# Optimization experiments

Hardware: AMD Instinct MI355X
Metric: run time of the kernel (lower is better)

Reference implementation:

```python
import jax, jax.numpy as jnp
import numpy as np

NEG = -10000.0
SINK = 16  # first 16 keys are always-attended sink tokens


def setup_inputs() -> dict:
    key = jax.random.key(0)
    k0, k1, k2 = jax.random.split(key, 3)
    B, H, KH, S, D = 1, 16, 4, 2048, 128
    return {
        "query": jax.random.normal(k0, (B, H, S, D), dtype=jnp.float32),
        "key_t": jax.random.normal(k1, (B, KH, S, D), dtype=jnp.float32),
        "value": jax.random.normal(k2, (B, KH, S, D), dtype=jnp.float32),
        "lsh_threshold": jnp.full((KH,), 70.0, dtype=jnp.float32),
        "top_k": 64,
        "window_size": 128,
    }


def reference(query, key_t, value, lsh_threshold, top_k, window_size):
    # query: [B,H,S,D]; key_t/value: [B,KH,S,D] (GQA, QH = H//KH)
    B, H, S, D = query.shape
    KH = key_t.shape[1]
    QH = H // KH
    q = query.reshape(B, KH, QH, S, D)

    # LSH sign-bit matching count. packbits64(x>=0) + (D - xor_popcount) ==
    # number of positions where sign(q)==sign(k) == (D + <sgn(q),sgn(k)>)/2.
    qs = jnp.where(q >= 0, 1.0, -1.0).astype(jnp.float32)
    ksgn = jnp.where(key_t >= 0, 1.0, -1.0).astype(jnp.float32)
    match = (D + jnp.einsum('bkqsd,bkld->bkqsl', qs, ksgn)) * 0.5  # [B,KH,QH,S,S]
    # max over the QH group (dim=2, keepdim) then compare against per-KV-head threshold
    lsh_mask = match.max(axis=2, keepdims=True) > lsh_threshold.reshape(1, KH, 1, 1, 1)

    qi = jnp.arange(S)[:, None]
    ki = jnp.arange(S)[None, :]
    causal = qi >= ki                                             # [S,S]
    window = ((jnp.abs(qi - ki) < window_size) | (ki < SINK)) & causal

    mask = causal & lsh_mask                                      # [B,KH,QH,S,S]

    scale = 1.0 / jnp.sqrt(jnp.asarray(D, jnp.float32))
    scores = jnp.einsum('bkqsd,bkld->bkqsl', q, key_t) * scale    # [B,KH,QH,S,S]
    scores = jnp.where(jnp.logical_not(mask) & jnp.logical_not(window), NEG, scores)

    # long-term candidates: exclude the local window, then take top_k per query row
    scores_lt = jnp.where(window, NEG, scores)
    _, idx = jax.lax.top_k(scores_lt, top_k)                      # [B,KH,QH,S,top_k]
    topk_mask = jnp.put_along_axis(
        jnp.zeros(scores.shape, dtype=bool), idx, True, axis=-1, inplace=False)

    both = window | topk_mask
    probs = jax.nn.softmax(jnp.where(both, scores, NEG), axis=-1)
    out = jnp.einsum('bkqsl,bkld->bskqd', probs, value)           # [B,S,KH,QH,D]
    return out.reshape(B, S, H * D)
```

## Files before the change

### kernel.cpp

```cpp
#include <hip/hip_runtime.h>

#define S_LEN   2048
#define D_DIM   128
#define KH_N    4
#define QH_N    4
#define H_N     (KH_N * QH_N)
#define SINK_N  16
#define SB_N    4
#define NREG    16
#define CHUNK   512
#define NCH     4
#define PLANE32 260
#define SCR32   672
#define TIECAP  672

typedef __attribute__((ext_vector_type(8))) _Float16 f16x8;
typedef __attribute__((ext_vector_type(2))) _Float16 f16x2;
typedef __attribute__((ext_vector_type(4))) float f32x4;

__device__ __forceinline__ void lds_fence() {
  asm volatile("s_waitcnt lgkmcnt(0)" ::: "memory");
}
__device__ __forceinline__ unsigned short f2h(float f) {
  _Float16 h = (_Float16)f;
  return __builtin_bit_cast(unsigned short, h);
}
__device__ __forceinline__ unsigned int pkrtz_u32(float a, float b) {
  return __builtin_bit_cast(unsigned int, __builtin_amdgcn_cvt_pkrtz(a, b));
}
__device__ __forceinline__ unsigned int pack_okey16(float a, float b) {
  unsigned int u = pkrtz_u32(a, b);
  unsigned int t = (u >> 15) & 0x00010001u;
  return u ^ ((t * 0x7FFFu) | 0x80008000u);
}
__device__ __forceinline__ float okinv16(unsigned int k) {
  unsigned short bits = (k & 0x8000u) ? (unsigned short)(k & 0x7FFFu)
                                      : (unsigned short)(~k & 0xFFFFu);
  return (float)__builtin_bit_cast(_Float16, bits);
}

__global__ __launch_bounds__(256) void pack_kernel(
    const float* __restrict__ k, const float* __restrict__ v,
    unsigned long long* __restrict__ signs,
    unsigned short* __restrict__ kf16, unsigned int* __restrict__ vf16) {
  const int wid  = (blockIdx.x * 256 + threadIdx.x) >> 6;
  const int lane = threadIdx.x & 63;
  const int rbase = wid * 4;
  const int KROWS = KH_N * S_LEN;

  if (rbase < KROWS) {
    const float* src = k + (size_t)rbase * D_DIM;
    float a[4], b[4];
#pragma unroll
    for (int r = 0; r < 4; r++) {
      a[r] = src[r * D_DIM + lane];
      b[r] = src[r * D_DIM + 64 + lane];
    }
#pragma unroll
    for (int r = 0; r < 4; r++) {
      unsigned long long b0 = __ballot(a[r] >= 0.0f);
      unsigned long long b1 = __ballot(b[r] >= 0.0f);
      if (lane == 0) {
        signs[(size_t)(rbase + r) * 2]     = b0;
        signs[(size_t)(rbase + r) * 2 + 1] = b1;
      }
      unsigned short* rb = kf16 + (size_t)(rbase + r) * 128;
      rb[lane]      = f2h(a[r]);
      rb[64 + lane] = f2h(b[r]);
    }
  } else {
    int vr = rbase - KROWS;
    const float* src = v + (size_t)vr * D_DIM;
    float2 f2[4];
#pragma unroll
    for (int r = 0; r < 4; r++)
      f2[r] = *(const float2*)(src + r * D_DIM + lane * 2);
#pragma unroll
    for (int r = 0; r < 4; r++) {
      unsigned int pk = (unsigned int)f2h(f2[r].x) |
                        ((unsigned int)f2h(f2[r].y) << 16);
      vf16[(size_t)(vr + r) * 64 + lane] = pk;
    }
  }
}

__global__ __launch_bounds__(512, 4) void attn_kernel(
    const float* __restrict__ query, const float* __restrict__ thr,
    const int* __restrict__ p_topk, const int* __restrict__ p_wsz,
    const unsigned long long* __restrict__ signs,
    const unsigned short* __restrict__ kf16,
    const unsigned int* __restrict__ vf16,
    float* __restrict__ out) {
  const int xcd  = blockIdx.x & 7;
  const int kh   = xcd >> 1;
  const int g    = ((blockIdx.x >> 3) << 1) | (xcd & 1);
  const int sb   = (511 - g) << 2;
  const int tid  = threadIdx.x;
  const int lane = tid & 63;
  const int w    = tid >> 6;
  const int col  = lane & 15;
  const int quad = lane >> 4;
  const int s_off = w >> 1;
  const int part  = w & 1;

  __shared__ __align__(16) unsigned int   buf[16 * PLANE32];
  __shared__ __align__(16) unsigned int   scr[8][SCR32];
  __shared__ __align__(16) unsigned short q_f16[16][136];
  __shared__ unsigned long long mask_sh[SB_N][32];
  __shared__ unsigned long long qs_sh[16][2];
  __shared__ int ncand_sh[SB_N];

  const int   topk   = *p_topk;
  const int   wsz    = *p_wsz;
  const float thresh = thr[kh];
  const float scale  = 0.088388347648318447f;

  const int s_w     = sb + s_off;
  const int nrows_w = s_w + 1;
  int wlo_w = s_w - (wsz - 1); if (wlo_w < 0) wlo_w = 0;
  const int lt_hi_w = s_w - wsz;
  const int imax_w  = (nrows_w + 127) >> 7;
  const int smax    = sb + 3;
  const int nrows_pad = (smax + 1 + 15) & ~15;

#pragma unroll
  for (int v = 0; v < 4; v++) {
    int r = v * 4 + (tid >> 7);
    int d = tid & 127;
    float f = query[((size_t)(kh * QH_N + (r & 3)) * S_LEN
                     + (sb + (r >> 2))) * D_DIM + d];
    unsigned long long b = __ballot(f >= 0.0f);
    if (lane == 0) qs_sh[v * 4 + (w >> 1)][w & 1] = b;
    q_f16[r][d] = f2h(f * scale);
  }
  if (tid < 128) mask_sh[tid >> 5][tid & 31] = 0ull;
  if (tid < SB_N) ncand_sh[tid] = 0;
  __syncthreads();

  {
    unsigned long long a0[4], a1[4];
#pragma unroll
    for (int q2 = 0; q2 < 4; q2++) {
      a0[q2] = qs_sh[s_off * 4 + q2][0];
      a1[q2] = qs_sh[s_off * 4 + q2][1];
    }
    const unsigned long long* ksg = signs + (size_t)kh * S_LEN * 2;
    int cnt = 0;
    for (int l0 = part * 64; l0 <= lt_hi_w; l0 += 128) {
      int l = l0 + lane;
      bool match = false;
      if (l >= SINK_N && l <= lt_hi_w) {
        ulonglong2 kk = *(const ulonglong2*)(ksg + 2 * l);
        int best = 0;
#pragma unroll
        for (int q2 = 0; q2 < 4; q2++) {
          int m = 128 - __popcll(a0[q2] ^ kk.x) - __popcll(a1[q2] ^ kk.y);
          best = best > m ? best : m;
        }
        match = ((float)best > thresh);
      }
      unsigned long long m = __ballot(match);
      if (lane == 0) mask_sh[s_off][l0 >> 6] = m;
      cnt += (int)__popcll(m);
    }
    if (lane == 0 && cnt) atomicAdd(&ncand_sh[s_off], cnt);
  }

  f16x8 bfrag[4];
#pragma unroll
  for (int ks = 0; ks < 4; ks++)
    bfrag[ks] = *(const f16x8*)&q_f16[col][ks * 32 + quad * 8];

  const unsigned short* kf_h = kf16 + ((size_t)kh << 11) * 128;
  unsigned int creg[2][NREG];
#pragma unroll
  for (int hq = 0; hq < 2; hq++)
#pragma unroll
    for (int i = 0; i < NREG; i++) creg[hq][i] = 0u;

#pragma unroll
  for (int cb = 0; cb < NCH; cb++) {
    int cbase = cb * CHUNK;
    int chunk_n = nrows_pad - cbase;
    if (chunk_n > CHUNK) chunk_n = CHUNK;
    if (chunk_n > 0) {
      int ntiles = chunk_n >> 4;
      for (int t = w; t < ntiles; t += 8) {
        int tb = cbase + t * 16;
        const unsigned char* ab =
            (const unsigned char*)(kf_h + (size_t)(tb + col) * 128) + quad * 16;
        f16x8 a0 = *(const f16x8*)(ab + 0);
        f16x8 a1 = *(const f16x8*)(ab + 64);
        f16x8 a2 = *(const f16x8*)(ab + 128);
        f16x8 a3 = *(const f16x8*)(ab + 192);
        f32x4 acc = {0.f, 0.f, 0.f, 0.f};
        acc = __builtin_amdgcn_mfma_f32_16x16x32_f16(a0, bfrag[0], acc, 0, 0, 0);
        acc = __builtin_amdgcn_mfma_f32_16x16x32_f16(a1, bfrag[1], acc, 0, 0, 0);
        acc = __builtin_amdgcn_mfma_f32_16x16x32_f16(a2, bfrag[2], acc, 0, 0, 0);
        acc = __builtin_amdgcn_mfma_f32_16x16x32_f16(a3, bfrag[3], acc, 0, 0, 0);
        unsigned int k01 = pack_okey16(acc[0], acc[1]);
        unsigned int k23 = pack_okey16(acc[2], acc[3]);
        int off = ((tb - cbase) >> 1) + quad * 2;
        buf[col * PLANE32 + off]     = k01;
        buf[col * PLANE32 + off + 1] = k23;
      }
    }
    __syncthreads();
    if (chunk_n > 0) {
#pragma unroll
      for (int hq = 0; hq < 2; hq++)
#pragma unroll
        for (int j2 = 0; j2 < 4; j2++) {
          int m = j2 * 64 + lane;
          if (2 * m < chunk_n)
            creg[hq][cb * 4 + j2] = buf[(2 * w + hq) * PLANE32 + m];
        }
    }
    __syncthreads();
  }

  unsigned int mybits = 0;
#pragma unroll
  for (int i = 0; i < NREG; i++) {
    if (i >= imax_w) break;
    unsigned long long wd = mask_sh[s_off][2 * i + (lane >> 5)];
    mybits |= ((unsigned int)((wd >> ((2 * lane) & 63)) & 3ull)) << (2 * i);
  }
  const int nc = ncand_sh[s_off];
  const bool selAll = (nc <= topk);

  unsigned int*       histw = &scr[w][0];
  unsigned long long* selq  = (unsigned long long*)&scr[w][256];
  unsigned int*       tls   = &scr[w][0];

  const int sub = lane & 15;
  const int quarter = lane >> 4;
  const uint4* vb4 = (const uint4*)(vf16 + ((size_t)kh << 11) * 64);

#pragma unroll
  for (int hq = 0; hq < 2; hq++) {
    const int qh = 2 * part + hq;

    unsigned int mx16 = 0;
#pragma unroll
    for (int i = 0; i < NREG; i++) {
      if (i >= imax_w) break;
      unsigned int u = creg[hq][i];
      int e0 = i * 128 + 2 * lane;
      unsigned int h0 = u & 0xFFFFu, h1 = u >> 16;
      if (e0 < nrows_w && h0 > mx16) mx16 = h0;
      if (e0 + 1 < nrows_w && h1 > mx16) mx16 = h1;
    }
#pragma unroll
    for (int off = 32; off > 0; off >>= 1) {
      unsigned int t = __shfl_down(mx16, off);
      mx16 = t > mx16 ? t : mx16;
    }
    mx16 = __shfl(mx16, 0);
    const float mxf = okinv16(mx16);

    unsigned int tkey = 0;
    bool useTie = false;
    int l_cut = S_LEN;
    if (!selAll) {
      unsigned int prefix = 0;
      int want = topk;
      unsigned int ceq = 0;
#pragma unroll
      for (int pass = 0; pass < 2; pass++) {
        int sh = 8 - pass * 8;
        {
          uint4 z = {0u, 0u, 0u, 0u};
          *(uint4*)&histw[lane * 4] = z;
        }
        lds_fence();
#pragma unroll
        for (int i = 0; i < NREG; i++) {
          if (i >= imax_w) break;
          unsigned int u = creg[hq][i];
          unsigned int b2 = (mybits >> (2 * i)) & 3u;
          if (b2 & 1u) {
            unsigned int key = u & 0xFFFFu;
            if ((pass == 0) || ((key >> 8) == prefix))
              atomicAdd(&histw[(key >> sh) & 255u], 1u);
          }
          if (b2 & 2u) {
            unsigned int key = u >> 16;
            if ((pass == 0) || ((key >> 8) == prefix))
              atomicAdd(&histw[(key >> sh) & 255u], 1u);
          }
        }
        lds_fence();
        uint4 cc = *(const uint4*)&histw[lane * 4];
        unsigned int c0 = cc.x, c1 = cc.y, c2 = cc.z, c3 = cc.w;
        unsigned int S3 = c3, S2 = c2 + S3, S1 = c1 + S2, S0 = c0 + S1;
        unsigned int tot = S0;
        unsigned int suf = tot;
#pragma unroll
        for (int off = 1; off < 64; off <<= 1) {
          unsigned int t = __shfl_down(suf, off);
          if (lane + off < 64) suf += t;
        }
        unsigned long long mk = __ballot(suf >= (unsigned int)want);
        int L = 63 - __clzll(mk);
        unsigned int se = suf - tot;
        unsigned int s3 = S3 + se, s2 = S2 + se, s1 = S1 + se, s0 = S0 + se;
        int j; unsigned int above, csel;
        unsigned int w2 = (unsigned int)want;
        if (s3 >= w2)      { j = 3; above = s3 - c3; csel = c3; }
        else if (s2 >= w2) { j = 2; above = s2 - c2; csel = c2; }
        else if (s1 >= w2) { j = 1; above = s1 - c1; csel = c1; }
        else               { j = 0; above = s0 - c0; csel = c0; }
        int d_me = (lane << 2) | j;
        int wp_me = want - (int)above;
        int digit = __shfl(d_me, L);
        want = __shfl(wp_me, L);
        ceq = (unsigned int)__shfl((int)csel, L);
        prefix = (prefix << 8) | (unsigned int)digit;
      }
      tkey = prefix;
      int rem = want;
      if ((int)ceq > rem) {
        useTie = true;
        if ((int)ceq <= TIECAP) {
          int tb = 0;
#pragma unroll
          for (int i = 0; i < NREG; i++) {
            if (i >= imax_w) break;
            unsigned int u = creg[hq][i];
            unsigned int b2 = (mybits >> (2 * i)) & 3u;
            int e0 = i * 128 + 2 * lane;
#pragma unroll
            for (int h2 = 0; h2 < 2; h2++) {
              bool tied = false;
              if (b2 & (1u << h2)) {
                unsigned int key = h2 ? (u >> 16) : (u & 0xFFFFu);
                tied = (key == tkey);
              }
              unsigned long long m = __ballot(tied);
              if (tied) {
                int pos = tb + __popcll(m & ((1ull << lane) - 1ull));
                tls[pos] = (unsigned int)(e0 + h2);
              }
              tb += (int)__popcll(m);
            }
          }
          lds_fence();
          unsigned int lcut = (unsigned int)S_LEN;
          for (int i2 = lane; i2 < (int)ceq; i2 += 64) {
            unsigned int v2 = tls[i2];
            int rank = 0;
            for (int j3 = 0; j3 < (int)ceq; j3++) rank += (tls[j3] < v2);
            if (rank == rem - 1) lcut = v2;
          }
#pragma unroll
          for (int off = 32; off > 0; off >>= 1) {
            unsigned int t = __shfl_down(lcut, off);
            lcut = t < lcut ? t : lcut;
          }
          l_cut = (int)__shfl((int)lcut, 0);
        } else {
          int lo = SINK_N, hi = lt_hi_w;
          while (lo < hi) {
            int mid = (lo + hi) >> 1;
            int cn = 0;
#pragma unroll
            for (int i = 0; i < NREG; i++) {
              if (i >= imax_w) break;
              unsigned int u = creg[hq][i];
              unsigned int b2 = (mybits >> (2 * i)) & 3u;
              int e0 = i * 128 + 2 * lane;
#pragma unroll
              for (int h2 = 0; h2 < 2; h2++) {
                if (b2 & (1u << h2)) {
                  unsigned int key = h2 ? (u >> 16) : (u & 0xFFFFu);
                  cn += (key == tkey && (e0 + h2) <= mid);
                }
              }
            }
#pragma unroll
            for (int off = 32; off > 0; off >>= 1) cn += __shfl_down(cn, off);
            cn = __shfl(cn, 0);
            if (cn >= rem) hi = mid; else lo = mid + 1;
          }
          l_cut = lo;
        }
      }
    }

    float sum = 0.0f;
    int bse = 0;
#pragma unroll
    for (int i = 0; i < NREG; i++) {
      if (i >= imax_w) break;
      unsigned int u = creg[hq][i];
      int e0 = i * 128 + 2 * lane;
#pragma unroll
      for (int h2 = 0; h2 < 2; h2++) {
        int e = e0 + h2;
        bool act = false;
        float p = 0.f;
        if (e < nrows_w) {
          unsigned int key = h2 ? (u >> 16) : (u & 0xFFFFu);
          bool inc = (e < SINK_N) || (e >= wlo_w);
          if (!inc && ((mybits >> (2 * i + h2)) & 1u))
            inc = selAll || (key > tkey) ||
                  (key == tkey && (!useTie || e <= l_cut));
          if (inc) { act = true; p = __expf(okinv16(key) - mxf); sum += p; }
        }
        unsigned long long m = __ballot(act);
        if (act) {
          int pi = bse + __popcll(m & ((1ull << lane) - 1ull));
          selq[pi] = ((unsigned long long)e << 32) |
                     (unsigned long long)__float_as_uint(p);
        }
        bse += (int)__popcll(m);
      }
    }
#pragma unroll
    for (int off = 32; off > 0; off >>= 1) sum += __shfl_down(sum, off);
    sum = __shfl(sum, 0);
    float rinv = 1.0f / sum;

    int nsel = bse;
    int nsel16 = (nsel + 15) & ~15;
    if (lane < nsel16 - nsel) selq[nsel + lane] = 0ull;
    lds_fence();

    float av[8] = {0.f, 0.f, 0.f, 0.f, 0.f, 0.f, 0.f, 0.f};
    for (int e = 0; e < nsel16; e += 16) {
      const unsigned long long* sq = &selq[e + 4 * quarter];
      ulonglong2 spA = *(const ulonglong2*)(sq);
      ulonglong2 spB = *(const ulonglong2*)(sq + 2);
      int l0 = (int)(spA.x >> 32), l1 = (int)(spA.y >> 32);
      int l2 = (int)(spB.x >> 32), l3 = (int)(spB.y >> 32);
      uint4 v0 = vb4[(size_t)l0 * 16 + sub];
      uint4 v1 = vb4[(size_t)l1 * 16 + sub];
      uint4 v2 = vb4[(size_t)l2 * 16 + sub];
      uint4 v3 = vb4[(size_t)l3 * 16 + sub];
      f16x2 phA = __builtin_bit_cast(
          f16x2, pkrtz_u32(__uint_as_float((unsigned int)spA.x),
                           __uint_as_float((unsigned int)spA.y)));
      f16x2 phB = __builtin_bit_cast(
          f16x2, pkrtz_u32(__uint_as_float((unsigned int)spB.x),
                           __uint_as_float((unsigned int)spB.y)));
#define DOT2P(va, vb, ph, comp, i0, i1)                                       \
      {                                                                       \
        unsigned int lo_ = __builtin_amdgcn_perm(vb.comp, va.comp, 0x05040100u); \
        unsigned int hi_ = __builtin_amdgcn_perm(vb.comp, va.comp, 0x07060302u); \
        av[i0] = __builtin_amdgcn_fdot2(__builtin_bit_cast(f16x2, lo_), ph,   \
                                        av[i0], false);                       \
        av[i1] = __builtin_amdgcn_fdot2(__builtin_bit_cast(f16x2, hi_), ph,   \
                                        av[i1], false);                       \
      }
      DOT2P(v0, v1, phA, x, 0, 1) DOT2P(v0, v1, phA, y, 2, 3)
      DOT2P(v0, v1, phA, z, 4, 5) DOT2P(v0, v1, phA, w, 6, 7)
      DOT2P(v2, v3, phB, x, 0, 1) DOT2P(v2, v3, phB, y, 2, 3)
      DOT2P(v2, v3, phB, z, 4, 5) DOT2P(v2, v3, phB, w, 6, 7)
#undef DOT2P
    }
#pragma unroll
    for (int d = 0; d < 8; d++) {
      av[d] += __shfl_xor(av[d], 16);
      av[d] += __shfl_xor(av[d], 32);
    }
    if (lane < 16) {
      size_t o = (size_t)s_w * (H_N * D_DIM)
               + (size_t)(kh * QH_N + qh) * D_DIM + (size_t)sub * 8;
      f32x4 r0 = {av[0] * rinv, av[1] * rinv, av[2] * rinv, av[3] * rinv};
      f32x4 r1 = {av[4] * rinv, av[5] * rinv, av[6] * rinv, av[7] * rinv};
      __builtin_nontemporal_store(r0, (f32x4*)(out + o));
      __builtin_nontemporal_store(r1, (f32x4*)(out + o + 4));
    }
    lds_fence();
  }
}

extern "C" void kernel_launch(void* const* d_in, const int* in_sizes, int n_in,
                              void* d_out, int out_size, void* d_ws, size_t ws_size,
                              hipStream_t stream) {
  const float* query = (const float*)d_in[0];
  const float* key   = (const float*)d_in[1];
  const float* value = (const float*)d_in[2];
  const float* thr   = (const float*)d_in[3];
  const int* p_topk  = (const int*)d_in[4];
  const int* p_wsz   = (const int*)d_in[5];
  float* out = (float*)d_out;

  char* ws = (char*)d_ws;
  unsigned long long* signs = (unsigned long long*)ws;
  unsigned short* kf16 = (unsigned short*)(ws + (size_t)KH_N * S_LEN * 16);
  unsigned int* vf16 = (unsigned int*)(ws + (size_t)KH_N * S_LEN * 16
                                          + (size_t)KH_N * S_LEN * 256);

  pack_kernel<<<1024, 256, 0, stream>>>(key, value, signs, kf16, vf16);

  attn_kernel<<<KH_N * (S_LEN / SB_N), 512, 0, stream>>>(
      query, thr, p_topk, p_wsz, signs, kf16, vf16, out);
}
```

Before: 275.9 us.

## Stage V chunks in LDS and gather selected rows from shared memory

Selected (index, prob) pairs are packed into 32-bit entries (16-bit index, fp16 prob), and per-128-row chunk offsets are recorded. The block then cooperatively stages each 128-row V chunk into LDS and every wave accumulates both query heads from the staged chunk. This replaces scattered global V gathers with coalesced loads that are shared across waves. It adds block-wide barriers per chunk, loads chunks that may be only sparsely used, lowers the tie-list cap and rounds the probabilities to fp16 earlier.

```diff
diff --git a/kernel.cpp b/kernel.cpp
--- a/kernel.cpp
+++ b/kernel.cpp
@@ -12,7 +12,7 @@
 #define NCH     4
 #define PLANE32 260
 #define SCR32   672
-#define TIECAP  672
+#define TIECAP  256
 
 typedef __attribute__((ext_vector_type(8))) _Float16 f16x8;
 typedef __attribute__((ext_vector_type(2))) _Float16 f16x2;
@@ -103,11 +103,12 @@
   const int s_off = w >> 1;
   const int part  = w & 1;
 
-  __shared__ __align__(16) unsigned int   buf[16 * PLANE32];
+  __shared__ __align__(16) unsigned int   big[8192];
   __shared__ __align__(16) unsigned int   scr[8][SCR32];
   __shared__ __align__(16) unsigned short q_f16[16][136];
   __shared__ unsigned long long mask_sh[SB_N][32];
   __shared__ unsigned long long qs_sh[16][2];
+  __shared__ unsigned short cse_sh[8][2][NREG + 1];
   __shared__ int ncand_sh[SB_N];
 
   const int   topk   = *p_topk;
@@ -201,8 +202,8 @@
         unsigned int k01 = pack_okey16(acc[0], acc[1]);
         unsigned int k23 = pack_okey16(acc[2], acc[3]);
         int off = ((tb - cbase) >> 1) + quad * 2;
-        buf[col * PLANE32 + off]     = k01;
-        buf[col * PLANE32 + off + 1] = k23;
+        big[col * PLANE32 + off]     = k01;
+        big[col * PLANE32 + off + 1] = k23;
       }
     }
     __syncthreads();
@@ -213,7 +214,7 @@
         for (int j2 = 0; j2 < 4; j2++) {
           int m = j2 * 64 + lane;
           if (2 * m < chunk_n)
-            creg[hq][cb * 4 + j2] = buf[(2 * w + hq) * PLANE32 + m];
+            creg[hq][cb * 4 + j2] = big[(2 * w + hq) * PLANE32 + m];
         }
     }
     __syncthreads();
@@ -229,17 +230,13 @@
   const int nc = ncand_sh[s_off];
   const bool selAll = (nc <= topk);
 
-  unsigned int*       histw = &scr[w][0];
-  unsigned long long* selq  = (unsigned long long*)&scr[w][256];
-  unsigned int*       tls   = &scr[w][0];
-
-  const int sub = lane & 15;
-  const int quarter = lane >> 4;
-  const uint4* vb4 = (const uint4*)(vf16 + ((size_t)kh << 11) * 64);
+  unsigned int* histw = &scr[w][0];
+
+  float rinv[2];
 
 #pragma unroll
   for (int hq = 0; hq < 2; hq++) {
-    const int qh = 2 * part + hq;
+    unsigned int* selq_h = &scr[w][256 + hq * 208];
 
     unsigned int mx16 = 0;
 #pragma unroll
@@ -323,6 +320,7 @@
       if ((int)ceq > rem) {
         useTie = true;
         if ((int)ceq <= TIECAP) {
+          unsigned int* tls = histw;
           int tb = 0;
 #pragma unroll
           for (int i = 0; i < NREG; i++) {
@@ -393,6 +391,7 @@
 #pragma unroll
     for (int i = 0; i < NREG; i++) {
       if (i >= imax_w) break;
+      if (lane == 0) cse_sh[w][hq][i] = (unsigned short)bse;
       unsigned int u = creg[hq][i];
       int e0 = i * 128 + 2 * lane;
 #pragma unroll
@@ -411,68 +410,91 @@
         unsigned long long m = __ballot(act);
         if (act) {
           int pi = bse + __popcll(m & ((1ull << lane) - 1ull));
-          selq[pi] = ((unsigned long long)e << 32) |
-                     (unsigned long long)__float_as_uint(p);
+          selq_h[pi] = ((unsigned int)e << 16) | (unsigned int)f2h(p);
         }
         bse += (int)__popcll(m);
       }
+    }
+    if (lane == 0) {
+      for (int i = imax_w; i <= NREG; i++)
+        cse_sh[w][hq][i] = (unsigned short)bse;
     }
 #pragma unroll
     for (int off = 32; off > 0; off >>= 1) sum += __shfl_down(sum, off);
     sum = __shfl(sum, 0);
-    float rinv = 1.0f / sum;
-
-    int nsel = bse;
-    int nsel16 = (nsel + 15) & ~15;
-    if (lane < nsel16 - nsel) selq[nsel + lane] = 0ull;
-    lds_fence();
-
-    float av[8] = {0.f, 0.f, 0.f, 0.f, 0.f, 0.f, 0.f, 0.f};
-    for (int e = 0; e < nsel16; e += 16) {
-      const unsigned long long* sq = &selq[e + 4 * quarter];
-      ulonglong2 spA = *(const ulonglong2*)(sq);
-      ulonglong2 spB = *(const ulonglong2*)(sq + 2);
-      int l0 = (int)(spA.x >> 32), l1 = (int)(spA.y >> 32);
-      int l2 = (int)(spB.x >> 32), l3 = (int)(spB.y >> 32);
-      uint4 v0 = vb4[(size_t)l0 * 16 + sub];
-      uint4 v1 = vb4[(size_t)l1 * 16 + sub];
-      uint4 v2 = vb4[(size_t)l2 * 16 + sub];
-      uint4 v3 = vb4[(size_t)l3 * 16 + sub];
-      f16x2 phA = __builtin_bit_cast(
-          f16x2, pkrtz_u32(__uint_as_float((unsigned int)spA.x),
-                           __uint_as_float((unsigned int)spA.y)));
-      f16x2 phB = __builtin_bit_cast(
-          f16x2, pkrtz_u32(__uint_as_float((unsigned int)spB.x),
-                           __uint_as_float((unsigned int)spB.y)));
+    rinv[hq] = 1.0f / sum;
+  }
+
+  const int sub = lane & 15;
+  const int quarter = lane >> 4;
+  const int nch_blk = (smax >> 7) + 1;
+  uint4* vstage = (uint4*)big;
+  const uint4* vsrc = (const uint4*)(vf16 + ((size_t)kh << 11) * 64);
+  float av[2][8];
+#pragma unroll
+  for (int hq = 0; hq < 2; hq++)
+#pragma unroll
+    for (int d = 0; d < 8; d++) av[hq][d] = 0.f;
+
+  for (int ch = 0; ch < nch_blk; ch++) {
+    __syncthreads();
+#pragma unroll
+    for (int k2 = 0; k2 < 4; k2++)
+      vstage[tid + k2 * 512] = vsrc[ch * 2048 + tid + k2 * 512];
+    __syncthreads();
+#pragma unroll
+    for (int hq = 0; hq < 2; hq++) {
+      const unsigned int* sq = &scr[w][256 + hq * 208];
+      int st = cse_sh[w][hq][ch];
+      int en = cse_sh[w][hq][ch + 1];
+      for (int base2 = st; base2 < en; base2 += 16) {
+        int sl = base2 + 4 * quarter;
+        unsigned int u0 = (sl + 0 < en) ? sq[sl + 0] : 0u;
+        unsigned int u1 = (sl + 1 < en) ? sq[sl + 1] : 0u;
+        unsigned int u2 = (sl + 2 < en) ? sq[sl + 2] : 0u;
+        unsigned int u3 = (sl + 3 < en) ? sq[sl + 3] : 0u;
+        uint4 v0 = vstage[(int)((u0 >> 16) & 127u) * 16 + sub];
+        uint4 v1 = vstage[(int)((u1 >> 16) & 127u) * 16 + sub];
+        uint4 v2 = vstage[(int)((u2 >> 16) & 127u) * 16 + sub];
+        uint4 v3 = vstage[(int)((u3 >> 16) & 127u) * 16 + sub];
+        f16x2 phA = __builtin_bit_cast(f16x2, (u0 & 0xFFFFu) | (u1 << 16));
+        f16x2 phB = __builtin_bit_cast(f16x2, (u2 & 0xFFFFu) | (u3 << 16));
 #define DOT2P(va, vb, ph, comp, i0, i1)                                       \
-      {                                                                       \
-        unsigned int lo_ = __builtin_amdgcn_perm(vb.comp, va.comp, 0x05040100u); \
-        unsigned int hi_ = __builtin_amdgcn_perm(vb.comp, va.comp, 0x07060302u); \
-        av[i0] = __builtin_amdgcn_fdot2(__builtin_bit_cast(f16x2, lo_), ph,   \
-                                        av[i0], false);                       \
-        av[i1] = __builtin_amdgcn_fdot2(__builtin_bit_cast(f16x2, hi_), ph,   \
-                                        av[i1], false);                       \
-      }
-      DOT2P(v0, v1, phA, x, 0, 1) DOT2P(v0, v1, phA, y, 2, 3)
-      DOT2P(v0, v1, phA, z, 4, 5) DOT2P(v0, v1, phA, w, 6, 7)
-      DOT2P(v2, v3, phB, x, 0, 1) DOT2P(v2, v3, phB, y, 2, 3)
-      DOT2P(v2, v3, phB, z, 4, 5) DOT2P(v2, v3, phB, w, 6, 7)
+        {                                                                     \
+          unsigned int lo_ = __builtin_amdgcn_perm(vb.comp, va.comp, 0x05040100u); \
+          unsigned int hi_ = __builtin_amdgcn_perm(vb.comp, va.comp, 0x07060302u); \
+          av[hq][i0] = __builtin_amdgcn_fdot2(__builtin_bit_cast(f16x2, lo_), \
+                                              ph, av[hq][i0], false);         \
+          av[hq][i1] = __builtin_amdgcn_fdot2(__builtin_bit_cast(f16x2, hi_), \
+                                              ph, av[hq][i1], false);         \
+        }
+        DOT2P(v0, v1, phA, x, 0, 1) DOT2P(v0, v1, phA, y, 2, 3)
+        DOT2P(v0, v1, phA, z, 4, 5) DOT2P(v0, v1, phA, w, 6, 7)
+        DOT2P(v2, v3, phB, x, 0, 1) DOT2P(v2, v3, phB, y, 2, 3)
+        DOT2P(v2, v3, phB, z, 4, 5) DOT2P(v2, v3, phB, w, 6, 7)
 #undef DOT2P
-    }
+      }
+    }
+  }
+
+#pragma unroll
+  for (int hq = 0; hq < 2; hq++) {
+    const int qh = 2 * part + hq;
 #pragma unroll
     for (int d = 0; d < 8; d++) {
-      av[d] += __shfl_xor(av[d], 16);
-      av[d] += __shfl_xor(av[d], 32);
+      av[hq][d] += __shfl_xor(av[hq][d], 16);
+      av[hq][d] += __shfl_xor(av[hq][d], 32);
     }
     if (lane < 16) {
       size_t o = (size_t)s_w * (H_N * D_DIM)
                + (size_t)(kh * QH_N + qh) * D_DIM + (size_t)sub * 8;
-      f32x4 r0 = {av[0] * rinv, av[1] * rinv, av[2] * rinv, av[3] * rinv};
-      f32x4 r1 = {av[4] * rinv, av[5] * rinv, av[6] * rinv, av[7] * rinv};
+      f32x4 r0 = {av[hq][0] * rinv[hq], av[hq][1] * rinv[hq],
+                  av[hq][2] * rinv[hq], av[hq][3] * rinv[hq]};
+      f32x4 r1 = {av[hq][4] * rinv[hq], av[hq][5] * rinv[hq],
+                  av[hq][6] * rinv[hq], av[hq][7] * rinv[hq]};
       __builtin_nontemporal_store(r0, (f32x4*)(out + o));
       __builtin_nontemporal_store(r1, (f32x4*)(out + o + 4));
     }
-    lds_fence();
   }
 }
 
```

Result: slower. 310.0 us (+12.3%).
